# Kernel optimization log

Hardware: AMD Instinct MI355X
Metric: run time of the kernel (lower is better)

The kernel has to match this reference:

```python
import jax, jax.numpy as jnp
import numpy as np

S = 1024        # img_size
RADIUS = 512    # number of radial bins
WEIGHT = 1.0


def _bin_idx():
    # Matches torch.meshgrid(arange(-s/2, s/2), ..., indexing='ij') with +0.5 offsets.
    xs = jnp.arange(-S / 2, S / 2, dtype=jnp.float32)
    d = jnp.sqrt((xs[:, None] + 0.5) ** 2 + (xs[None, :] + 0.5) ** 2)  # [S, S]
    # Bin edges are integers 0..RADIUS, so mask (d>=r)&(d<r+1) == (floor(d)==r).
    idx = jnp.floor(d).astype(jnp.int32)
    # Pixels with d >= RADIUS fall in no mask -> overflow bucket RADIUS (dropped later).
    return jnp.where(d < RADIUS, idx, RADIUS).reshape(-1)  # [S*S]


def _power_spec(image):
    ft = jnp.fft.fft2(image)                 # [B, C, S, S] complex
    return jnp.fft.fftshift(jnp.abs(ft) ** 2, axes=(-2, -1))


def _radial_power_spec(ps2d, idx):
    B, C = ps2d.shape[0], ps2d.shape[1]
    flat = ps2d.reshape(B * C, S * S)
    # Histogram reduction: O(S*S) instead of the original O(RADIUS*S*S) dense mask multiply.
    seg = jax.vmap(lambda v: jax.ops.segment_sum(v, idx, num_segments=RADIUS + 1))(flat)
    rad = seg[:, :RADIUS] / (S * S)          # mean over (H, W), drop overflow bucket
    return rad.reshape(B, C, RADIUS).sum(axis=1)  # sum over channel dim


def setup_inputs() -> dict:
    key = jax.random.key(0)
    k1, k2 = jax.random.split(key)
    output = jax.random.normal(k1, (16, 1, S, S), dtype=jnp.float32)
    target = jax.random.normal(k2, (16, 1, S, S), dtype=jnp.float32)
    return {"output": output, "target": target}


def reference(output, target):
    idx = _bin_idx()
    ps_out = _radial_power_spec(_power_spec(output), idx)   # [B, RADIUS]
    ps_tgt = _radial_power_spec(_power_spec(target), idx)   # [B, RADIUS]
    return jnp.mean(jnp.abs(ps_out - ps_tgt)) * WEIGHT
```

## Files before the change

kernel.cpp:

```cpp
#include <hip/hip_runtime.h>
#include <math.h>

#define S 1024
#define RADIUS 512
#define NIMG 32
#define RGROUP 16

__device__ __forceinline__ float2 cmul(float2 a, float2 b) {
    return make_float2(a.x * b.x - a.y * b.y, a.x * b.y + a.y * b.x);
}
__device__ __forceinline__ float2 cadd(float2 a, float2 b) { return make_float2(a.x + b.x, a.y + b.y); }
__device__ __forceinline__ float2 csub(float2 a, float2 b) { return make_float2(a.x - b.x, a.y - b.y); }

__device__ const float2 C16[8] = {
    {1.0f, 0.0f},
    {0.92387953251128674f, -0.38268343236508978f},
    {0.70710678118654757f, -0.70710678118654746f},
    {0.38268343236508984f, -0.92387953251128674f},
    {0.0f, -1.0f},
    {-0.38268343236508973f, -0.92387953251128674f},
    {-0.70710678118654746f, -0.70710678118654757f},
    {-0.92387953251128663f, -0.38268343236508989f},
};
__device__ const float2 C8T[4] = {
    {1.0f, 0.0f},
    {0.70710678118654757f, -0.70710678118654746f},
    {0.0f, -1.0f},
    {-0.70710678118654746f, -0.70710678118654757f},
};
__device__ const float2 W512T[8] = {
    {1.0f, 0.0f},
    {0.99992470183914454f, -0.012271538285719925f},
    {0.99969881869620425f, -0.024541228522912288f},
    {0.99932238458834954f, -0.036807222941358832f},
    {0.99879545620517241f, -0.049067674327418015f},
    {0.99811811290014918f, -0.061320736302208578f},
    {0.99729045667869021f, -0.073564563599667426f},
    {0.99631261218277800f, -0.085797312344439894f},
};
__device__ const float2 W64T[8] = {
    {1.0f, 0.0f},
    {0.99518472667219693f, -0.098017140329560604f},
    {0.98078528040323044f, -0.19509032201612825f},
    {0.95694033573220886f, -0.29028467725446233f},
    {0.92387953251128674f, -0.38268343236508978f},
    {0.88192126434835505f, -0.47139673682599764f},
    {0.83146961230254524f, -0.55557023301960218f},
    {0.77301045336273699f, -0.63439328416364549f},
};
__device__ const float2 W128P[8] = {
    {1.0f, 0.0f},
    {0.99879545620517241f, -0.049067674327418015f},
    {0.99518472667219693f, -0.098017140329560604f},
    {0.98917650996478101f, -0.14673047445536175f},
    {0.98078528040323044f, -0.19509032201612825f},
    {0.97003125319454397f, -0.24298017990326390f},
    {0.95694033573220886f, -0.29028467725446233f},
    {0.94154406518302081f, -0.33688985339222005f},
};
__device__ const float2 W1024P[8] = {
    {1.0f, 0.0f},
    {0.99998117528260111f, -0.0061358846491544753f},
    {0.99992470183914454f, -0.012271538285719925f},
    {0.99983058179582340f, -0.018406729905804820f},
    {0.99969881869620425f, -0.024541228522912288f},
    {0.99952941750109314f, -0.030674803176636626f},
    {0.99932238458834954f, -0.036807222941358832f},
    {0.99907772775264536f, -0.042938256934940820f},
};

__device__ __forceinline__ void fft16(float2 r[16], float2 T) {
    float2 tc[8];
    #pragma unroll
    for (int u = 0; u < 8; ++u) tc[u] = cmul(T, C16[u]);
    #pragma unroll
    for (int u = 0; u < 8; ++u) {
        float2 a = r[u], b = r[u + 8];
        r[u] = cadd(a, b);
        r[u + 8] = cmul(csub(a, b), tc[u]);
    }
    T = cmul(T, T);
    #pragma unroll
    for (int u = 0; u < 4; ++u) tc[u] = cmul(T, C16[2 * u]);
    #pragma unroll
    for (int g = 0; g < 2; ++g)
        #pragma unroll
        for (int u = 0; u < 4; ++u) {
            int lo = g * 8 + u;
            float2 a = r[lo], b = r[lo + 4];
            r[lo] = cadd(a, b);
            r[lo + 4] = cmul(csub(a, b), tc[u]);
        }
    T = cmul(T, T);
    #pragma unroll
    for (int u = 0; u < 2; ++u) tc[u] = cmul(T, C16[4 * u]);
    #pragma unroll
    for (int g = 0; g < 4; ++g)
        #pragma unroll
        for (int u = 0; u < 2; ++u) {
            int lo = g * 4 + u;
            float2 a = r[lo], b = r[lo + 2];
            r[lo] = cadd(a, b);
            r[lo + 2] = cmul(csub(a, b), tc[u]);
        }
    T = cmul(T, T);
    #pragma unroll
    for (int g = 0; g < 8; ++g) {
        int lo = g * 2;
        float2 a = r[lo], b = r[lo + 1];
        r[lo] = cadd(a, b);
        r[lo + 1] = cmul(csub(a, b), T);
    }
}

__device__ __forceinline__ void fft8(float2 r[8], float2 T) {
    float2 tc[4];
    #pragma unroll
    for (int u = 0; u < 4; ++u) tc[u] = cmul(T, C8T[u]);
    #pragma unroll
    for (int u = 0; u < 4; ++u) {
        float2 a = r[u], b = r[u + 4];
        r[u] = cadd(a, b);
        r[u + 4] = cmul(csub(a, b), tc[u]);
    }
    T = cmul(T, T);
    #pragma unroll
    for (int u = 0; u < 2; ++u) tc[u] = cmul(T, C8T[2 * u]);
    #pragma unroll
    for (int g = 0; g < 2; ++g)
        #pragma unroll
        for (int u = 0; u < 2; ++u) {
            int lo = g * 4 + u;
            float2 a = r[lo], b = r[lo + 2];
            r[lo] = cadd(a, b);
            r[lo + 2] = cmul(csub(a, b), tc[u]);
        }
    T = cmul(T, T);
    #pragma unroll
    for (int g = 0; g < 4; ++g) {
        int lo = g * 2;
        float2 a = r[lo], b = r[lo + 1];
        r[lo] = cadd(a, b);
        r[lo + 1] = cmul(csub(a, b), T);
    }
}

__device__ __forceinline__ void fft_last2(float2 r[16], int c) {
    #pragma unroll
    for (int m = 0; m < 16; ++m) {
        float vx = __shfl_xor(r[m].x, 2, 64);
        float vy = __shfl_xor(r[m].y, 2, 64);
        if (c & 2) {
            float dx = vx - r[m].x, dy = vy - r[m].y;
            if (c & 1) { r[m].x = dy; r[m].y = -dx; }
            else       { r[m].x = dx; r[m].y = dy; }
        } else {
            r[m].x += vx; r[m].y += vy;
        }
    }
    #pragma unroll
    for (int m = 0; m < 16; ++m) {
        float vx = __shfl_xor(r[m].x, 1, 64);
        float vy = __shfl_xor(r[m].y, 1, 64);
        if (c & 1) { r[m].x = vx - r[m].x; r[m].y = vy - r[m].y; }
        else       { r[m].x += vx; r[m].y += vy; }
    }
}

__device__ __forceinline__ int A1x(int n) {
    int j = n >> 6;
    return (n & ~63) | ((n & 63) ^ (j << 2));
}

__device__ __forceinline__ int bitrev3(int x) {
    return ((x & 1) << 2) | (x & 2) | ((x >> 2) & 1);
}

__global__ __launch_bounds__(512)
void fft_rows(const float* __restrict__ outp, const float* __restrict__ tgtp,
              float2* __restrict__ WpT, int imgBase) {
    __shared__ float2 buf[8 * 1024];
    const int t = threadIdx.x;
    const int w = t >> 6, tau = t & 63;
    const int yy = blockIdx.x * 8 + w;
    const int i = blockIdx.y, g = imgBase + i;
    const float* img = (g < 16 ? outp : tgtp) + (size_t)(g & 15) * S * S;
    const float* r0 = img + (size_t)(2 * yy) * S;
    const float* r1 = r0 + S;

    float2 r[16];
    #pragma unroll
    for (int j = 0; j < 16; ++j) r[j] = make_float2(r0[64 * j + tau], r1[64 * j + tau]);

    float2 T;
    { float sv, cv; sincosf(-6.283185307179586f * (float)tau / 1024.0f, &sv, &cv); T = make_float2(cv, sv); }
    fft16(r, T);

    float2* mybuf = buf + (w << 10);
    #pragma unroll
    for (int j = 0; j < 16; ++j) mybuf[A1x(64 * j + tau)] = r[j];
    const int b = tau >> 2, c = tau & 3;
    #pragma unroll
    for (int m = 0; m < 16; ++m) r[m] = mybuf[(b << 6) + 4 * (m ^ b) + c];

    { float sv, cv; sincosf(-6.283185307179586f * (float)c / 64.0f, &sv, &cv); T = make_float2(cv, sv); }
    fft16(r, T);
    fft_last2(r, c);

    #pragma unroll
    for (int m = 0; m < 16; ++m) {
        int n = (b << 6) + 4 * m + c;
        int k = (int)(__brev((unsigned)n) >> 22);
        mybuf[k ^ (w << 1)] = r[m];
    }
    __syncthreads();

    const int yy0 = blockIdx.x * 8;
    float2* dst = WpT + (size_t)i * 512 * 1024;
    #pragma unroll
    for (int q = 0; q < 16; ++q) {
        int idx = q * 512 + t;
        int uu = idx >> 3, wv = idx & 7;
        float2 val = buf[(wv << 10) | (uu ^ (wv << 1))];
        dst[(size_t)uu * 512 + yy0 + wv] = val;
    }
}

__global__ __launch_bounds__(512, 4)
void fft_cols_store(const float2* __restrict__ WpT, float* __restrict__ P, int imgBase) {
    __shared__ float2 tbuf[8 * 512];
    const int t = threadIdx.x;
    const int w = t >> 6, tau = t & 63;
    const int i = blockIdx.y;
    const int u = blockIdx.x * 4 + (w >> 1);
    const int setb = w & 1;
    const bool active = (u <= 512);

    const int b3 = tau >> 3, lam = tau & 7;
    float2 X[8];
    float2* mb = tbuf + (w << 9);

    if (active) {
        const float2* Wimg = WpT + (size_t)i * 512 * 1024;
        const int mu = (1024 - u) & 1023;
        const float2* rowA = Wimg + (size_t)u * 512;
        const float2* rowM = Wimg + (size_t)mu * 512;

        #pragma unroll
        for (int j = 0; j < 8; ++j) {
            float2 A = rowA[64 * j + tau];
            float2 M = rowM[64 * j + tau];
            X[j] = (setb == 0)
                 ? make_float2(0.5f * (A.x + M.x), 0.5f * (A.y - M.y))
                 : make_float2(0.5f * (A.y + M.y), 0.5f * (M.x - A.x));
        }

        fft8(X, cmul(W64T[b3], W512T[lam]));

        #pragma unroll
        for (int j = 0; j < 8; ++j) mb[(j << 6) | (tau ^ (j << 3) ^ j)] = X[j];
        #pragma unroll
        for (int c = 0; c < 8; ++c) X[c] = mb[(b3 << 6) | (((c ^ b3) << 3) | (lam ^ b3))];

        fft8(X, W64T[lam]);

        #pragma unroll
        for (int c = 0; c < 8; ++c) mb[(b3 << 6) | (((c ^ b3) << 3) | (lam ^ b3))] = X[c];
        #pragma unroll
        for (int d = 0; d < 8; ++d) X[d] = mb[(b3 << 6) | (((lam ^ b3) << 3) | (d ^ b3))];

        fft8(X, make_float2(1.0f, 0.0f));

        const int base9 = 8 * bitrev3(lam) + bitrev3(b3);
        #pragma unroll
        for (int d = 0; d < 8; ++d) {
            mb[(bitrev3(d) << 6) + base9] = X[d];
        }
    }
    __syncthreads();

    if (active) {
        const float2* b0 = tbuf + ((w & ~1) << 9);
        const float2* b1 = tbuf + ((w | 1) << 9);
        const float2 Wtau = cmul(W128P[tau >> 3], W1024P[tau & 7]);
        float* Pimg = P + (size_t)i * 1024 * 1024;
        const int um = (1024 - u) & 1023;

        #pragma unroll
        for (int m = 0; m < 8; ++m) {
            const int f = tau + 64 * m;
            float2 x0 = b0[f];
            float2 x1 = b1[f];
            float2 Wf = cmul(Wtau, C16[m]);
            float2 wx = cmul(Wf, x1);
            float2 G = (setb == 0) ? cadd(x0, wx)
                                   : csub(x0, wx);
            float p = G.x * G.x + G.y * G.y;
            const int v = f + (setb << 9);
            Pimg[(size_t)u * 1024 + v] = p;
            const int vm = (1024 - v) & 1023;
            Pimg[(size_t)um * 1024 + vm] = p;
        }
    }
}

__global__ __launch_bounds__(512)
void bin_scan(const float* __restrict__ P, float* __restrict__ partial, int imgBase) {
    __shared__ float pref[512];
    __shared__ float cws[8];
    __shared__ float cwx[8];
    const int t = threadIdx.x;
    const int lane = t & 63, w = t >> 6;
    const int i = blockIdx.y;
    const int g = imgBase + i;
    const int u0 = blockIdx.x * RGROUP;
    const float* Pimg = P + (size_t)i * 1024 * 1024;

    const int r = t;
    const float r2  = (float)(r * r);
    const float r12 = (float)((r + 1) * (r + 1));
    float acc = 0.0f;

    for (int k = 0; k < RGROUP; ++k) {
        const int u = u0 + k;
        const float* row = Pimg + (size_t)u * 1024;
        float F = row[t] + row[1023 - t];

        float s = F;
        #pragma unroll
        for (int off = 1; off < 64; off <<= 1) {
            float n = __shfl_up(s, off, 64);
            if (lane >= off) s += n;
        }
        pref[t] = s;
        if (lane == 63) cws[w] = s;
        __syncthreads();
        if (t < 8) {
            float x = 0.0f;
            #pragma unroll
            for (int j = 0; j < 8; ++j) {
                if (j < t) x += cws[j];
            }
            cwx[t] = x;
        }
        __syncthreads();

        const float cu = (u < 512) ? (u + 0.5f) : (u - 1023.5f);
        const float cu2 = cu * cu;
        const float Bv = r12 - cu2;
        if (Bv > 0.0f) {
            const float Av = r2 - cu2;
            float cvlo = (Av > 0.0f) ? sqrtf(Av) : 0.0f;
            float cvhi = sqrtf(Bv);
            int vlo = (int)ceilf(cvlo - 0.5f);
            int vhi = (int)ceilf(cvhi - 0.5f);
            if (vhi > 512) vhi = 512;
            if (vlo < 0) vlo = 0;
            if (vhi > vlo) {
                float hi = pref[vhi - 1] + cwx[(vhi - 1) >> 6];
                float lo = (vlo > 0) ? (pref[vlo - 1] + cwx[(vlo - 1) >> 6]) : 0.0f;
                acc += hi - lo;
            }
        }
        __syncthreads();
    }
    partial[(((size_t)g * 64) + blockIdx.x) * 512 + t] = acc;
}

__global__ __launch_bounds__(512)
void reduce_partials(const float* __restrict__ partial, float* __restrict__ rad) {
    const int g = blockIdx.x;
    const int t = threadIdx.x;
    const float* p = partial + (size_t)g * 64 * 512;
    float s = 0.0f;
    for (int b = 0; b < 64; ++b) s += p[(size_t)b * 512 + t];
    rad[(size_t)g * 512 + t] = s;
}

__global__ __launch_bounds__(256)
void final_loss(const float* __restrict__ rad, float* __restrict__ out) {
    __shared__ float red[256];
    const int t = threadIdx.x;
    float acc = 0.0f;
    for (int i = t; i < 16 * RADIUS; i += 256) {
        int bb = i >> 9;
        int rr = i & (RADIUS - 1);
        float o = rad[(size_t)bb * RADIUS + rr];
        float gg = rad[(size_t)(bb + 16) * RADIUS + rr];
        acc += fabsf(o - gg);
    }
    red[t] = acc;
    __syncthreads();
    for (int off = 128; off > 0; off >>= 1) {
        if (t < off) red[t] += red[t + off];
        __syncthreads();
    }
    if (t == 0) {
        out[0] = red[0] / ((float)S * (float)S) / (16.0f * (float)RADIUS);
    }
}

extern "C" void kernel_launch(void* const* d_in, const int* in_sizes, int n_in,
                              void* d_out, int out_size, void* d_ws, size_t ws_size,
                              hipStream_t stream) {
    const float* outp = (const float*)d_in[0];
    const float* tgtp = (const float*)d_in[1];
    float* dout = (float*)d_out;

    char* ws = (char*)d_ws;
    float* rad = (float*)ws;
    const size_t partBytes = (size_t)NIMG * 64 * 512 * sizeof(float);
    float* partial = (float*)(ws + 65536);
    const size_t wptBytes = (size_t)512 * 1024 * sizeof(float2);
    const size_t pBytes   = (size_t)1024 * 1024 * sizeof(float);
    size_t used = 65536 + partBytes;
    size_t avail = (ws_size > used) ? (ws_size - used) : 0;
    int chunk = (int)(avail / (wptBytes + pBytes));
    if (chunk > NIMG) chunk = NIMG;
    if (chunk < 1) chunk = 1;

    float2* WpT = (float2*)(ws + used);
    float*  P   = (float*)(ws + used + (size_t)chunk * wptBytes);

    for (int base = 0; base < NIMG; base += chunk) {
        int c = (NIMG - base < chunk) ? (NIMG - base) : chunk;
        fft_rows<<<dim3(64, c), 512, 0, stream>>>(outp, tgtp, WpT, base);
        fft_cols_store<<<dim3(129, c), 512, 0, stream>>>(WpT, P, base);
        bin_scan<<<dim3(64, c), 512, 0, stream>>>(P, partial, base);
    }

    reduce_partials<<<NIMG, 512, 0, stream>>>(partial, rad);
    final_loss<<<1, 256, 0, stream>>>(rad, dout);
}
```

Before: 191.2 us.

## Fuse column FFT with radial binning to skip full power-spectrum round trip

Merges the column FFT and the radial-bin scan into one kernel. Each block now bins its own 4 rows and their Hermitian mirror rows straight from shared memory instead of writing the full 1024x1024 power spectrum to global memory and reading it back. Twiddle factors in fft_rows also come from the existing lookup tables instead of sincosf. The cost is more partial rows to reduce (129 per image instead of 64) and extra syncs and shared memory per block, which may lower occupancy.

New measurement: 171.5 us. -10.3%, faster.

```diff
diff --git a/kernel.cpp b/kernel.cpp
--- a/kernel.cpp
+++ b/kernel.cpp
@@ -4,7 +4,7 @@
 #define S 1024
 #define RADIUS 512
 #define NIMG 32
-#define RGROUP 16
+#define PBX 129
 
 __device__ __forceinline__ float2 cmul(float2 a, float2 b) {
     return make_float2(a.x * b.x - a.y * b.y, a.x * b.y + a.y * b.x);
@@ -192,8 +192,7 @@
     #pragma unroll
     for (int j = 0; j < 16; ++j) r[j] = make_float2(r0[64 * j + tau], r1[64 * j + tau]);
 
-    float2 T;
-    { float sv, cv; sincosf(-6.283185307179586f * (float)tau / 1024.0f, &sv, &cv); T = make_float2(cv, sv); }
+    float2 T = cmul(W128P[tau >> 3], W1024P[tau & 7]);
     fft16(r, T);
 
     float2* mybuf = buf + (w << 10);
@@ -203,8 +202,7 @@
     #pragma unroll
     for (int m = 0; m < 16; ++m) r[m] = mybuf[(b << 6) + 4 * (m ^ b) + c];
 
-    { float sv, cv; sincosf(-6.283185307179586f * (float)c / 64.0f, &sv, &cv); T = make_float2(cv, sv); }
-    fft16(r, T);
+    fft16(r, W64T[c]);
     fft_last2(r, c);
 
     #pragma unroll
@@ -227,12 +225,16 @@
 }
 
 __global__ __launch_bounds__(512, 4)
-void fft_cols_store(const float2* __restrict__ WpT, float* __restrict__ P, int imgBase) {
+void fft_cols_bin2(const float2* __restrict__ WpT, float* __restrict__ partial, int imgBase) {
     __shared__ float2 tbuf[8 * 512];
+    __shared__ float pref[512];
+    __shared__ float cws[8];
+    __shared__ float cwx[8];
     const int t = threadIdx.x;
     const int w = t >> 6, tau = t & 63;
-    const int i = blockIdx.y;
-    const int u = blockIdx.x * 4 + (w >> 1);
+    const int i = blockIdx.y, g = imgBase + i;
+    const int l = w >> 1;
+    const int u = blockIdx.x * 4 + l;
     const int setb = w & 1;
     const bool active = (u <= 512);
 
@@ -279,13 +281,11 @@
     }
     __syncthreads();
 
+    float p[8];
     if (active) {
         const float2* b0 = tbuf + ((w & ~1) << 9);
         const float2* b1 = tbuf + ((w | 1) << 9);
         const float2 Wtau = cmul(W128P[tau >> 3], W1024P[tau & 7]);
-        float* Pimg = P + (size_t)i * 1024 * 1024;
-        const int um = (1024 - u) & 1023;
-
         #pragma unroll
         for (int m = 0; m < 8; ++m) {
             const int f = tau + 64 * m;
@@ -295,45 +295,45 @@
             float2 wx = cmul(Wf, x1);
             float2 G = (setb == 0) ? cadd(x0, wx)
                                    : csub(x0, wx);
-            float p = G.x * G.x + G.y * G.y;
-            const int v = f + (setb << 9);
-            Pimg[(size_t)u * 1024 + v] = p;
-            const int vm = (1024 - v) & 1023;
-            Pimg[(size_t)um * 1024 + vm] = p;
-        }
-    }
-}
-
-__global__ __launch_bounds__(512)
-void bin_scan(const float* __restrict__ P, float* __restrict__ partial, int imgBase) {
-    __shared__ float pref[512];
-    __shared__ float cws[8];
-    __shared__ float cwx[8];
-    const int t = threadIdx.x;
-    const int lane = t & 63, w = t >> 6;
-    const int i = blockIdx.y;
-    const int g = imgBase + i;
-    const int u0 = blockIdx.x * RGROUP;
-    const float* Pimg = P + (size_t)i * 1024 * 1024;
+            p[m] = G.x * G.x + G.y * G.y;
+        }
+    }
+    __syncthreads();
+
+    float* Prow = (float*)tbuf;
+    if (active) {
+        #pragma unroll
+        for (int m = 0; m < 8; ++m) {
+            const int v = tau + 64 * m + (setb << 9);
+            Prow[(l << 10) + v] = p[m];
+        }
+    }
+    __syncthreads();
 
     const int r = t;
     const float r2  = (float)(r * r);
     const float r12 = (float)((r + 1) * (r + 1));
     float acc = 0.0f;
 
-    for (int k = 0; k < RGROUP; ++k) {
-        const int u = u0 + k;
-        const float* row = Pimg + (size_t)u * 1024;
-        float F = row[t] + row[1023 - t];
-
+    for (int rowi = 0; rowi < 8; ++rowi) {
+        const int ll = rowi >> 1;
+        const int mir = rowi & 1;
+        const int uu = blockIdx.x * 4 + ll;
+        const bool valid = (uu <= 512) && (!mir || (uu >= 1 && uu <= 511));
+        float F = 0.0f;
+        if (valid) {
+            const float* PR = Prow + (ll << 10);
+            F = mir ? (PR[t + 1] + PR[(1024 - t) & 1023])
+                    : (PR[t] + PR[1023 - t]);
+        }
         float s = F;
         #pragma unroll
         for (int off = 1; off < 64; off <<= 1) {
             float n = __shfl_up(s, off, 64);
-            if (lane >= off) s += n;
+            if (tau >= off) s += n;
         }
         pref[t] = s;
-        if (lane == 63) cws[w] = s;
+        if (tau == 63) cws[w] = s;
         __syncthreads();
         if (t < 8) {
             float x = 0.0f;
@@ -344,36 +344,38 @@
             cwx[t] = x;
         }
         __syncthreads();
-
-        const float cu = (u < 512) ? (u + 0.5f) : (u - 1023.5f);
-        const float cu2 = cu * cu;
-        const float Bv = r12 - cu2;
-        if (Bv > 0.0f) {
-            const float Av = r2 - cu2;
-            float cvlo = (Av > 0.0f) ? sqrtf(Av) : 0.0f;
-            float cvhi = sqrtf(Bv);
-            int vlo = (int)ceilf(cvlo - 0.5f);
-            int vhi = (int)ceilf(cvhi - 0.5f);
-            if (vhi > 512) vhi = 512;
-            if (vlo < 0) vlo = 0;
-            if (vhi > vlo) {
-                float hi = pref[vhi - 1] + cwx[(vhi - 1) >> 6];
-                float lo = (vlo > 0) ? (pref[vlo - 1] + cwx[(vlo - 1) >> 6]) : 0.0f;
-                acc += hi - lo;
+        if (valid) {
+            const float cuv = mir ? ((float)uu - 0.5f)
+                                  : ((uu < 512) ? ((float)uu + 0.5f) : 511.5f);
+            const float cu2 = cuv * cuv;
+            const float Bv = r12 - cu2;
+            if (Bv > 0.0f) {
+                const float Av = r2 - cu2;
+                float cvlo = (Av > 0.0f) ? sqrtf(Av) : 0.0f;
+                float cvhi = sqrtf(Bv);
+                int vlo = (int)ceilf(cvlo - 0.5f);
+                int vhi = (int)ceilf(cvhi - 0.5f);
+                if (vhi > 512) vhi = 512;
+                if (vlo < 0) vlo = 0;
+                if (vhi > vlo) {
+                    float hi = pref[vhi - 1] + cwx[(vhi - 1) >> 6];
+                    float lo = (vlo > 0) ? (pref[vlo - 1] + cwx[(vlo - 1) >> 6]) : 0.0f;
+                    acc += hi - lo;
+                }
             }
         }
         __syncthreads();
     }
-    partial[(((size_t)g * 64) + blockIdx.x) * 512 + t] = acc;
+    partial[(((size_t)g * PBX) + blockIdx.x) * 512 + t] = acc;
 }
 
 __global__ __launch_bounds__(512)
 void reduce_partials(const float* __restrict__ partial, float* __restrict__ rad) {
     const int g = blockIdx.x;
     const int t = threadIdx.x;
-    const float* p = partial + (size_t)g * 64 * 512;
+    const float* p = partial + (size_t)g * PBX * 512;
     float s = 0.0f;
-    for (int b = 0; b < 64; ++b) s += p[(size_t)b * 512 + t];
+    for (int b = 0; b < PBX; ++b) s += p[(size_t)b * 512 + t];
     rad[(size_t)g * 512 + t] = s;
 }
 
@@ -409,24 +411,20 @@
 
     char* ws = (char*)d_ws;
     float* rad = (float*)ws;
-    const size_t partBytes = (size_t)NIMG * 64 * 512 * sizeof(float);
+    const size_t partBytes = (size_t)NIMG * PBX * 512 * sizeof(float);
     float* partial = (float*)(ws + 65536);
-    const size_t wptBytes = (size_t)512 * 1024 * sizeof(float2);
-    const size_t pBytes   = (size_t)1024 * 1024 * sizeof(float);
+    float2* WpT = (float2*)(ws + 65536 + partBytes);
+    const size_t perImg = (size_t)512 * 1024 * sizeof(float2);
     size_t used = 65536 + partBytes;
     size_t avail = (ws_size > used) ? (ws_size - used) : 0;
-    int chunk = (int)(avail / (wptBytes + pBytes));
+    int chunk = (int)(avail / perImg);
     if (chunk > NIMG) chunk = NIMG;
     if (chunk < 1) chunk = 1;
-
-    float2* WpT = (float2*)(ws + used);
-    float*  P   = (float*)(ws + used + (size_t)chunk * wptBytes);
 
     for (int base = 0; base < NIMG; base += chunk) {
         int c = (NIMG - base < chunk) ? (NIMG - base) : chunk;
         fft_rows<<<dim3(64, c), 512, 0, stream>>>(outp, tgtp, WpT, base);
-        fft_cols_store<<<dim3(129, c), 512, 0, stream>>>(WpT, P, base);
-        bin_scan<<<dim3(64, c), 512, 0, stream>>>(P, partial, base);
+        fft_cols_bin2<<<dim3(PBX, c), 512, 0, stream>>>(WpT, partial, base);
     }
 
     reduce_partials<<<NIMG, 512, 0, stream>>>(partial, rad);
```
